# Optimization experiments

Measured on AMD Instinct MI355X. Metric: run time of the kernel, lower is better.

## Reference

```python
import jax, jax.numpy as jnp
from jax import lax
import numpy as np

B, T, IN, H = 8192, 512, 5, 32


def setup_inputs() -> dict:
    key = jax.random.key(0)
    ks = jax.random.split(key, 7)
    s_ih = 1.0 / np.sqrt(H)
    return {
        "x": jax.random.normal(ks[0], (B, T, IN), dtype=jnp.float32),
        "W_ih": jax.random.normal(ks[1], (4 * H, IN), dtype=jnp.float32) * s_ih,
        "W_hh": jax.random.normal(ks[2], (4 * H, H), dtype=jnp.float32) * s_ih,
        "b_ih": jax.random.normal(ks[3], (4 * H,), dtype=jnp.float32) * s_ih,
        "b_hh": jax.random.normal(ks[4], (4 * H,), dtype=jnp.float32) * s_ih,
        "W_fc": jax.random.normal(ks[5], (1, H), dtype=jnp.float32) * s_ih,
        "b_fc": jax.random.normal(ks[6], (1,), dtype=jnp.float32) * s_ih,
    }


def reference(x, W_ih, W_hh, b_ih, b_hh, W_fc, b_fc):
    # x: [B, T, IN]. Single-layer batch-first LSTM (PyTorch gate order i,f,g,o),
    # then linear head on the final timestep's hidden state.
    b = x.shape[0]
    h0 = jnp.zeros((b, H), x.dtype)
    c0 = jnp.zeros((b, H), x.dtype)
    # Precompute input projections for all timesteps in one GEMM: [T, B, 4H]
    x_t = jnp.swapaxes(x, 0, 1)  # [T, B, IN]
    x_proj = jnp.einsum("tbi,gi->tbg", x_t, W_ih) + b_ih + b_hh

    def step(carry, xp):
        h, c = carry
        gates = xp + h @ W_hh.T  # [B, 4H]
        i, f, g, o = jnp.split(gates, 4, axis=-1)
        i = jax.nn.sigmoid(i)
        f = jax.nn.sigmoid(f)
        g = jnp.tanh(g)
        o = jax.nn.sigmoid(o)
        c = f * c + i * g
        h = o * jnp.tanh(c)
        return (h, c), None

    (h_last, _), _ = lax.scan(step, (h0, c0), x_proj)
    return h_last @ W_fc.T + b_fc  # [B, 1]
```

## Files before the change

kernel.cpp:

```cpp
#include <hip/hip_runtime.h>


typedef __attribute__((ext_vector_type(8))) short short8;
typedef __attribute__((ext_vector_type(4))) float f32x4;
typedef __attribute__((ext_vector_type(4))) unsigned int u32x4;

static constexpr int BB  = 8192;
static constexpr int TT  = 512;
static constexpr int NIN = 5;
static constexpr int HH  = 32;

__device__ __forceinline__ unsigned short bf_rne(float f) {
    unsigned int u = __float_as_uint(f);
    u = (u + 0x7FFFu + ((u >> 16) & 1u)) >> 16;
    return (unsigned short)u;
}
__device__ __forceinline__ float bf_f32(unsigned short h) {
    return __uint_as_float((unsigned int)h << 16);
}
__device__ __forceinline__ float fast_sigmoid(float x) {
    float e = __builtin_amdgcn_exp2f(-1.4426950408889634f * x);
    return __builtin_amdgcn_rcpf(1.0f + e);
}
__device__ __forceinline__ float fast_tanh(float x) {
    float e = __builtin_amdgcn_exp2f(2.8853900817779268f * x);
    return 1.0f - 2.0f * __builtin_amdgcn_rcpf(1.0f + e);
}

__global__ __launch_bounds__(64) void lstm_wave(
    const float* __restrict__ x,
    const float* __restrict__ W_ih,
    const float* __restrict__ W_hh,
    const float* __restrict__ b_ih,
    const float* __restrict__ b_hh,
    const float* __restrict__ W_fc,
    const float* __restrict__ b_fc,
    float* __restrict__ out)
{
    const int lane = threadIdx.x & 63;
    const int col  = lane & 15;
    const int kg   = lane >> 4;
    const int b0   = blockIdx.x * 8;
    const int bloc = col & 7;
    const bool jlow = (col < 8);
    const int jbase = 4 * kg + (jlow ? 0 : 16);

    short8 Ahh_hi[8], Ahh_lo[8], Ax[8];
#pragma unroll
    for (int t4 = 0; t4 < 8; ++t4) {
        const int gr = 16 * t4 + col;
#pragma unroll
        for (int e = 0; e < 8; ++e) {
            float wv = W_hh[gr * HH + kg * 8 + e];
            unsigned short hi = bf_rne(wv);
            Ahh_hi[t4][e] = (short)hi;
            Ahh_lo[t4][e] = (short)bf_rne(wv - bf_f32(hi));
        }
        float bias = b_ih[gr] + b_hh[gr];
        unsigned short bh_ = bf_rne(bias);
        unsigned short bl_ = bf_rne(bias - bf_f32(bh_));
        short8 v;
#pragma unroll
        for (int e = 0; e < 8; ++e) v[e] = 0;
        if (kg == 0 || kg == 1) {
#pragma unroll
            for (int e = 0; e < NIN; ++e) v[e] = (short)bf_rne(W_ih[gr * NIN + e]);
            v[5] = (short)((kg == 0) ? bh_ : bl_);
        } else if (kg == 2) {
#pragma unroll
            for (int e = 0; e < NIN; ++e) {
                float wv = W_ih[gr * NIN + e];
                unsigned short h2 = bf_rne(wv);
                v[e] = (short)bf_rne(wv - bf_f32(h2));
            }
        }
        Ax[t4] = v;
    }

    const int xb = (lane / 5 < 8) ? (lane / 5) : 7;
    int xe = lane - 5 * xb; if (xe > 4) xe = 4;
    const float* px = x + ((size_t)(b0 + xb) * TT) * NIN + xe;

    const unsigned shx  = (kg == 1) ? 16u : 0u;
    const unsigned mskx = (kg == 3) ? 0u : 0xFFFFu;
    const unsigned one5 = (kg < 2) ? (0x3F80u << 16) : 0u;

    const int srcA = 32 * (kg & 1) + bloc + 8 * (kg >> 1);
    const int srcB = srcA + 16;

    float xv = px[0]; px += NIN;
    unsigned int xpk = 0;
    {
        unsigned short hi = bf_rne(xv);
        unsigned short lo = bf_rne(xv - bf_f32(hi));
        xpk = (unsigned int)hi | ((unsigned int)lo << 16);
    }

    unsigned int bh0 = 0, bh1 = 0, bh2 = 0, bh3 = 0;
    float c0 = 0.f, c1 = 0.f, c2 = 0.f, c3 = 0.f;
    float h0 = 0.f, h1 = 0.f, h2 = 0.f, h3 = 0.f;

    const f32x4 z = {0.f, 0.f, 0.f, 0.f};

#pragma unroll 1
    for (int t = 0; t < TT; ++t) {
        float xvn = xv;
        if (t + 1 < TT) { xvn = px[0]; px += NIN; }

        unsigned int p0x = (unsigned)__shfl((int)xpk, 5 * bloc + 0, 64);
        unsigned int p1x = (unsigned)__shfl((int)xpk, 5 * bloc + 1, 64);
        unsigned int p2x = (unsigned)__shfl((int)xpk, 5 * bloc + 2, 64);
        unsigned int p3x = (unsigned)__shfl((int)xpk, 5 * bloc + 3, 64);
        unsigned int p4x = (unsigned)__shfl((int)xpk, 5 * bloc + 4, 64);
        unsigned int a0 = (p0x >> shx) & mskx;
        unsigned int a1 = (p1x >> shx) & mskx;
        unsigned int a2 = (p2x >> shx) & mskx;
        unsigned int a3 = (p3x >> shx) & mskx;
        unsigned int a4 = (p4x >> shx) & mskx;
        u32x4 bxu = {a0 | (a1 << 16), a2 | (a3 << 16), a4 | one5, 0u};
        short8 bx = __builtin_bit_cast(short8, bxu);
        u32x4 bhu = {bh0, bh1, bh2, bh3};
        short8 bh = __builtin_bit_cast(short8, bhu);

        f32x4 acc[8];
#pragma unroll
        for (int t4 = 0; t4 < 8; ++t4)
            acc[t4] = __builtin_amdgcn_mfma_f32_16x16x32_bf16(Ahh_lo[t4], bh, z, 0, 0, 0);
#pragma unroll
        for (int t4 = 0; t4 < 8; ++t4)
            acc[t4] = __builtin_amdgcn_mfma_f32_16x16x32_bf16(Ahh_hi[t4], bh, acc[t4], 0, 0, 0);
#pragma unroll
        for (int t4 = 0; t4 < 8; ++t4)
            acc[t4] = __builtin_amdgcn_mfma_f32_16x16x32_bf16(Ax[t4], bx, acc[t4], 0, 0, 0);

#pragma unroll
        for (int r = 0; r < 4; ++r) {
            float gi = jlow ? acc[0][r] : acc[1][r];
            float gf = jlow ? acc[2][r] : acc[3][r];
            float gg = jlow ? acc[4][r] : acc[5][r];
            float go = jlow ? acc[6][r] : acc[7][r];
            float iv = fast_sigmoid(gi);
            float fv = fast_sigmoid(gf);
            float gv = fast_tanh(gg);
            float ov = fast_sigmoid(go);
            float cc = (r == 0 ? c0 : r == 1 ? c1 : r == 2 ? c2 : c3);
            cc = fv * cc + iv * gv;
            float hh = ov * fast_tanh(cc);
            if (r == 0) { c0 = cc; h0 = hh; }
            else if (r == 1) { c1 = cc; h1 = hh; }
            else if (r == 2) { c2 = cc; h2 = hh; }
            else { c3 = cc; h3 = hh; }
        }

        unsigned int p0 = (unsigned int)bf_rne(h0) | ((unsigned int)bf_rne(h1) << 16);
        unsigned int p1 = (unsigned int)bf_rne(h2) | ((unsigned int)bf_rne(h3) << 16);
        bh0 = (unsigned)__shfl((int)p0, srcA, 64);
        bh1 = (unsigned)__shfl((int)p1, srcA, 64);
        bh2 = (unsigned)__shfl((int)p0, srcB, 64);
        bh3 = (unsigned)__shfl((int)p1, srcB, 64);

        {
            unsigned short hi = bf_rne(xvn);
            unsigned short lo = bf_rne(xvn - bf_f32(hi));
            xpk = (unsigned int)hi | ((unsigned int)lo << 16);
        }
        xv = xvn;
    }

    float v = h0 * W_fc[jbase + 0] + h1 * W_fc[jbase + 1]
            + h2 * W_fc[jbase + 2] + h3 * W_fc[jbase + 3];
    v += __shfl_xor(v, 8);
    v += __shfl_xor(v, 16);
    v += __shfl_xor(v, 32);
    if (lane < 8) out[b0 + lane] = v + b_fc[0];
}

extern "C" void kernel_launch(void* const* d_in, const int* in_sizes, int n_in,
                              void* d_out, int out_size, void* d_ws, size_t ws_size,
                              hipStream_t stream) {
    const float* x    = (const float*)d_in[0];
    const float* W_ih = (const float*)d_in[1];
    const float* W_hh = (const float*)d_in[2];
    const float* b_ih = (const float*)d_in[3];
    const float* b_hh = (const float*)d_in[4];
    const float* W_fc = (const float*)d_in[5];
    const float* b_fc = (const float*)d_in[6];
    float* out = (float*)d_out;

    lstm_wave<<<dim3(BB / 8), dim3(64), 0, stream>>>(
        x, W_ih, W_hh, b_ih, b_hh, W_fc, b_fc, out);
}
```

Baseline: 330.2 us.

## Switch LSTM recurrence to single-pass fp16 MFMA and precompute next input projection

Replaces the split bf16 hi/lo weight scheme (three MFMA passes per step) with a single fp16 MFMA pass for the recurrent product. The input projection for step t+1 is computed off the critical path, so it overlaps with the current step's gate math. Each lane now loads the x values directly instead of using five shuffles per step. This cuts the MFMA count on the serial dependency chain from 24 to 8 per step, at the cost of fp16 precision for weights and hidden state, with possible accuracy loss.

```diff
diff --git a/kernel.cpp b/kernel.cpp
--- a/kernel.cpp
+++ b/kernel.cpp
@@ -1,7 +1,7 @@
 #include <hip/hip_runtime.h>
 
 
-typedef __attribute__((ext_vector_type(8))) short short8;
+typedef __attribute__((ext_vector_type(8))) _Float16 half8;
 typedef __attribute__((ext_vector_type(4))) float f32x4;
 typedef __attribute__((ext_vector_type(4))) unsigned int u32x4;
 
@@ -10,13 +10,9 @@
 static constexpr int NIN = 5;
 static constexpr int HH  = 32;
 
-__device__ __forceinline__ unsigned short bf_rne(float f) {
-    unsigned int u = __float_as_uint(f);
-    u = (u + 0x7FFFu + ((u >> 16) & 1u)) >> 16;
-    return (unsigned short)u;
-}
-__device__ __forceinline__ float bf_f32(unsigned short h) {
-    return __uint_as_float((unsigned int)h << 16);
+__device__ __forceinline__ unsigned short f16b(float f) {
+    _Float16 h = (_Float16)f;
+    return __builtin_bit_cast(unsigned short, h);
 }
 __device__ __forceinline__ float fast_sigmoid(float x) {
     float e = __builtin_amdgcn_exp2f(-1.4426950408889634f * x);
@@ -27,7 +23,7 @@
     return 1.0f - 2.0f * __builtin_amdgcn_rcpf(1.0f + e);
 }
 
-__global__ __launch_bounds__(64) void lstm_wave(
+__global__ __launch_bounds__(64) void lstm_f16(
     const float* __restrict__ x,
     const float* __restrict__ W_ih,
     const float* __restrict__ W_hh,
@@ -45,93 +41,74 @@
     const bool jlow = (col < 8);
     const int jbase = 4 * kg + (jlow ? 0 : 16);
 
-    short8 Ahh_hi[8], Ahh_lo[8], Ax[8];
+    half8 Ahh[8], Ax[8];
 #pragma unroll
     for (int t4 = 0; t4 < 8; ++t4) {
         const int gr = 16 * t4 + col;
 #pragma unroll
-        for (int e = 0; e < 8; ++e) {
-            float wv = W_hh[gr * HH + kg * 8 + e];
-            unsigned short hi = bf_rne(wv);
-            Ahh_hi[t4][e] = (short)hi;
-            Ahh_lo[t4][e] = (short)bf_rne(wv - bf_f32(hi));
-        }
-        float bias = b_ih[gr] + b_hh[gr];
-        unsigned short bh_ = bf_rne(bias);
-        unsigned short bl_ = bf_rne(bias - bf_f32(bh_));
-        short8 v;
+        for (int e = 0; e < 8; ++e)
+            Ahh[t4][e] = (_Float16)W_hh[gr * HH + kg * 8 + e];
+        half8 v;
 #pragma unroll
-        for (int e = 0; e < 8; ++e) v[e] = 0;
-        if (kg == 0 || kg == 1) {
+        for (int e = 0; e < 8; ++e) v[e] = (_Float16)0.f;
+        if (kg == 0) {
 #pragma unroll
-            for (int e = 0; e < NIN; ++e) v[e] = (short)bf_rne(W_ih[gr * NIN + e]);
-            v[5] = (short)((kg == 0) ? bh_ : bl_);
-        } else if (kg == 2) {
-#pragma unroll
-            for (int e = 0; e < NIN; ++e) {
-                float wv = W_ih[gr * NIN + e];
-                unsigned short h2 = bf_rne(wv);
-                v[e] = (short)bf_rne(wv - bf_f32(h2));
-            }
+            for (int e = 0; e < NIN; ++e) v[e] = (_Float16)W_ih[gr * NIN + e];
+            float bias = b_ih[gr] + b_hh[gr];
+            _Float16 bh_ = (_Float16)bias;
+            v[5] = bh_;
+            v[6] = (_Float16)(bias - (float)bh_);
         }
         Ax[t4] = v;
     }
 
-    const int xb = (lane / 5 < 8) ? (lane / 5) : 7;
-    int xe = lane - 5 * xb; if (xe > 4) xe = 4;
-    const float* px = x + ((size_t)(b0 + xb) * TT) * NIN + xe;
-
-    const unsigned shx  = (kg == 1) ? 16u : 0u;
-    const unsigned mskx = (kg == 3) ? 0u : 0xFFFFu;
-    const unsigned one5 = (kg < 2) ? (0x3F80u << 16) : 0u;
-
     const int srcA = 32 * (kg & 1) + bloc + 8 * (kg >> 1);
     const int srcB = srcA + 16;
 
-    float xv = px[0]; px += NIN;
-    unsigned int xpk = 0;
-    {
-        unsigned short hi = bf_rne(xv);
-        unsigned short lo = bf_rne(xv - bf_f32(hi));
-        xpk = (unsigned int)hi | ((unsigned int)lo << 16);
-    }
+    const bool xk = (kg == 0);
+
+    const float* px = x + (size_t)(b0 + bloc) * TT * NIN;
+    float x0 = px[0], x1 = px[1], x2 = px[2], x3 = px[3], x4 = px[4];
 
     unsigned int bh0 = 0, bh1 = 0, bh2 = 0, bh3 = 0;
     float c0 = 0.f, c1 = 0.f, c2 = 0.f, c3 = 0.f;
     float h0 = 0.f, h1 = 0.f, h2 = 0.f, h3 = 0.f;
+    const f32x4 z = {0.f, 0.f, 0.f, 0.f};
 
-    const f32x4 z = {0.f, 0.f, 0.f, 0.f};
+    auto make_bx = [&](float v0, float v1, float v2, float v3, float v4) -> half8 {
+        unsigned w0 = (unsigned)f16b(v0) | ((unsigned)f16b(v1) << 16);
+        unsigned w1 = (unsigned)f16b(v2) | ((unsigned)f16b(v3) << 16);
+        unsigned w2 = (unsigned)f16b(v4) | (0x3C00u << 16);
+        unsigned w3 = 0x00003C00u;
+        u32x4 u = {xk ? w0 : 0u, xk ? w1 : 0u, xk ? w2 : 0u, xk ? w3 : 0u};
+        return __builtin_bit_cast(half8, u);
+    };
+
+    f32x4 accN[8];
+    {
+        half8 bx0 = make_bx(x0, x1, x2, x3, x4);
+#pragma unroll
+        for (int t4 = 0; t4 < 8; ++t4)
+            accN[t4] = __builtin_amdgcn_mfma_f32_16x16x32_f16(Ax[t4], bx0, z, 0, 0, 0);
+    }
 
 #pragma unroll 1
     for (int t = 0; t < TT; ++t) {
-        float xvn = xv;
-        if (t + 1 < TT) { xvn = px[0]; px += NIN; }
+        const size_t off = (size_t)((t + 1 < TT) ? (t + 1) : t) * NIN;
+        float n0 = px[off + 0], n1 = px[off + 1], n2 = px[off + 2],
+              n3 = px[off + 3], n4 = px[off + 4];
 
-        unsigned int p0x = (unsigned)__shfl((int)xpk, 5 * bloc + 0, 64);
-        unsigned int p1x = (unsigned)__shfl((int)xpk, 5 * bloc + 1, 64);
-        unsigned int p2x = (unsigned)__shfl((int)xpk, 5 * bloc + 2, 64);
-        unsigned int p3x = (unsigned)__shfl((int)xpk, 5 * bloc + 3, 64);
-        unsigned int p4x = (unsigned)__shfl((int)xpk, 5 * bloc + 4, 64);
-        unsigned int a0 = (p0x >> shx) & mskx;
-        unsigned int a1 = (p1x >> shx) & mskx;
-        unsigned int a2 = (p2x >> shx) & mskx;
-        unsigned int a3 = (p3x >> shx) & mskx;
-        unsigned int a4 = (p4x >> shx) & mskx;
-        u32x4 bxu = {a0 | (a1 << 16), a2 | (a3 << 16), a4 | one5, 0u};
-        short8 bx = __builtin_bit_cast(short8, bxu);
         u32x4 bhu = {bh0, bh1, bh2, bh3};
-        short8 bh = __builtin_bit_cast(short8, bhu);
-
+        half8 bh = __builtin_bit_cast(half8, bhu);
         f32x4 acc[8];
 #pragma unroll
         for (int t4 = 0; t4 < 8; ++t4)
-            acc[t4] = __builtin_amdgcn_mfma_f32_16x16x32_bf16(Ahh_lo[t4], bh, z, 0, 0, 0);
+            acc[t4] = __builtin_amdgcn_mfma_f32_16x16x32_f16(Ahh[t4], bh, accN[t4], 0, 0, 0);
+
+        half8 bxn = make_bx(n0, n1, n2, n3, n4);
 #pragma unroll
         for (int t4 = 0; t4 < 8; ++t4)
-            acc[t4] = __builtin_amdgcn_mfma_f32_16x16x32_bf16(Ahh_hi[t4], bh, acc[t4], 0, 0, 0);
-#pragma unroll
-        for (int t4 = 0; t4 < 8; ++t4)
-            acc[t4] = __builtin_amdgcn_mfma_f32_16x16x32_bf16(Ax[t4], bx, acc[t4], 0, 0, 0);
+            accN[t4] = __builtin_amdgcn_mfma_f32_16x16x32_f16(Ax[t4], bxn, z, 0, 0, 0);
 
 #pragma unroll
         for (int r = 0; r < 4; ++r) {
@@ -144,7 +121,7 @@
             float gv = fast_tanh(gg);
             float ov = fast_sigmoid(go);
             float cc = (r == 0 ? c0 : r == 1 ? c1 : r == 2 ? c2 : c3);
-            cc = fv * cc + iv * gv;
+            cc = fmaf(fv, cc, iv * gv);
             float hh = ov * fast_tanh(cc);
             if (r == 0) { c0 = cc; h0 = hh; }
             else if (r == 1) { c1 = cc; h1 = hh; }
@@ -152,19 +129,14 @@
             else { c3 = cc; h3 = hh; }
         }
 
-        unsigned int p0 = (unsigned int)bf_rne(h0) | ((unsigned int)bf_rne(h1) << 16);
-        unsigned int p1 = (unsigned int)bf_rne(h2) | ((unsigned int)bf_rne(h3) << 16);
+        unsigned int p0 = (unsigned)f16b(h0) | ((unsigned)f16b(h1) << 16);
+        unsigned int p1 = (unsigned)f16b(h2) | ((unsigned)f16b(h3) << 16);
         bh0 = (unsigned)__shfl((int)p0, srcA, 64);
         bh1 = (unsigned)__shfl((int)p1, srcA, 64);
         bh2 = (unsigned)__shfl((int)p0, srcB, 64);
         bh3 = (unsigned)__shfl((int)p1, srcB, 64);
 
-        {
-            unsigned short hi = bf_rne(xvn);
-            unsigned short lo = bf_rne(xvn - bf_f32(hi));
-            xpk = (unsigned int)hi | ((unsigned int)lo << 16);
-        }
-        xv = xvn;
+        x0 = n0; x1 = n1; x2 = n2; x3 = n3; x4 = n4;
     }
 
     float v = h0 * W_fc[jbase + 0] + h1 * W_fc[jbase + 1]
@@ -187,6 +159,6 @@
     const float* b_fc = (const float*)d_in[6];
     float* out = (float*)d_out;
 
-    lstm_wave<<<dim3(BB / 8), dim3(64), 0, stream>>>(
+    lstm_f16<<<dim3(BB / 8), dim3(64), 0, stream>>>(
         x, W_ih, W_hh, b_ih, b_hh, W_fc, b_fc, out);
 }
```

After: 270.8 us (median of 2 runs). -18.0%, faster.
